# Kernel tuning notes

Hardware: AMD Instinct MI355X
Metric: run time of the kernel (lower is better)

## Reference

```python
import jax, jax.numpy as jnp
import numpy as np
from jax import lax

B, T, C = 32, 4096, 128
CLAMP_LO, CLAMP_HI = 1e-4, 1.0 - 1e-4
LOGIT_ALPHA0 = 0.0                 # logit(0.5)
LOGIT_BETA0 = float(np.log(0.1 / 0.9))  # logit(0.1)


def setup_inputs() -> dict:
    key = jax.random.key(0)
    x = jax.random.normal(key, (B, T, C), dtype=jnp.float32)
    logit_alpha = jnp.full((C,), LOGIT_ALPHA0, dtype=jnp.float32)
    logit_beta = jnp.full((C,), LOGIT_BETA0, dtype=jnp.float32)
    return {"x": x, "logit_alpha": logit_alpha, "logit_beta": logit_beta}


def reference(x, logit_alpha, logit_beta):
    # Holt level+slope exponential smoothing; output is the level series.
    a = jnp.clip(jax.nn.sigmoid(logit_alpha), CLAMP_LO, CLAMP_HI).astype(x.dtype)  # [C]
    b = jnp.clip(jax.nn.sigmoid(logit_beta), CLAMP_LO, CLAMP_HI).astype(x.dtype)   # [C]

    L0 = x[:, 0, :]                       # [B, C]
    slope0 = jnp.zeros_like(L0)

    def step(carry, xt):
        L_prev, slope = carry
        pred = L_prev + slope
        L = pred + a * (xt - pred)
        slope = slope + b * (L - L_prev - slope)
        return (L, slope), L

    xs = jnp.moveaxis(x[:, 1:, :], 1, 0)  # [T-1, B, C], time-major for scan
    _, Ls = lax.scan(step, (L0, slope0), xs)
    out = jnp.concatenate([L0[:, None, :], jnp.moveaxis(Ls, 0, 1)], axis=1)  # [B, T, C]
    return out
```

## Files before the change

kernel.cpp:

```cpp
#include <hip/hip_runtime.h>
#include <math.h>


#define B_ 32
#define T_ 4096
#define C_ 128
#define K_ 64
#define S_ (T_ / K_)
#define C2 (C_ / 2)
#define NCHUNK (B_ * K_)
#define BATCH 16

typedef float v2f __attribute__((ext_vector_type(2)));

__device__ __forceinline__ float sig_clamp(float z) {
    float s = 1.0f / (1.0f + expf(-z));
    return fminf(fmaxf(s, 1.0e-4f), 1.0f - 1.0e-4f);
}

#define STEP(xv0, xv1)                                   \
    {                                                    \
        const float p0 = L0 + sl0;                       \
        const float p1 = L1 + sl1;                       \
        const float g0 = a0 * ((xv0) - p0);              \
        const float g1 = a1 * ((xv1) - p1);              \
        L0 = p0 + g0;  sl0 = fmaf(b0, g0, sl0);          \
        L1 = p1 + g1;  sl1 = fmaf(b1, g1, sl1);          \
    }

__global__ __launch_bounds__(256, 2) void p1_offsets(
        const float* __restrict__ x,
        const float* __restrict__ logit_alpha,
        const float* __restrict__ logit_beta,
        float4* __restrict__ w) {
    const int tid = threadIdx.x & 63;
    const int chunk = blockIdx.x * 4 + (threadIdx.x >> 6);
    const int b = chunk >> 6;
    const int k = chunk & (K_ - 1);

    const float2 la2 = ((const float2*)logit_alpha)[tid];
    const float2 lb2 = ((const float2*)logit_beta)[tid];
    const float a0 = sig_clamp(la2.x), a1 = sig_clamp(la2.y);
    const float b0 = sig_clamp(lb2.x), b1 = sig_clamp(lb2.y);

    const float2* xp = (const float2*)x + ((size_t)b * T_ + (size_t)k * S_) * C2 + tid;

    float2 buf[BATCH];
    float L0, sl0 = 0.0f, L1, sl1 = 0.0f;

    #pragma unroll
    for (int i = 0; i < BATCH; ++i) buf[i] = xp[(size_t)i * C2];
    if (k == 0) { L0 = buf[0].x; L1 = buf[0].y; }
    else        { L0 = 0.0f;     L1 = 0.0f;     }
    #pragma unroll
    for (int i = 0; i < BATCH; ++i) STEP(buf[i].x, buf[i].y);

    for (int base = BATCH; base < S_; base += BATCH) {
        #pragma unroll
        for (int i = 0; i < BATCH; ++i) buf[i] = xp[(size_t)(base + i) * C2];
        #pragma unroll
        for (int i = 0; i < BATCH; ++i) STEP(buf[i].x, buf[i].y);
    }

    w[(size_t)chunk * 64 + tid] = make_float4(L0, sl0, L1, sl1);
}

__global__ __launch_bounds__(256, 2) void p2_emit(
        const float* __restrict__ x,
        const float* __restrict__ logit_alpha,
        const float* __restrict__ logit_beta,
        const float4* __restrict__ w,
        float* __restrict__ out) {
    const int tid = threadIdx.x & 63;
    const int chunk = (NCHUNK - 1) - (blockIdx.x * 4 + (threadIdx.x >> 6));
    const int b = chunk >> 6;
    const int k = chunk & (K_ - 1);

    const float2 la2 = ((const float2*)logit_alpha)[tid];
    const float2 lb2 = ((const float2*)logit_beta)[tid];
    const float a0 = sig_clamp(la2.x), a1 = sig_clamp(la2.y);
    const float b0 = sig_clamp(lb2.x), b1 = sig_clamp(lb2.y);

    const size_t off = ((size_t)b * T_ + (size_t)k * S_) * C2 + tid;
    const v2f* xp = (const v2f*)x + off;
    v2f* op = (v2f*)out + off;

    float L0, sl0 = 0.0f, L1, sl1 = 0.0f;

    if (k > 0) {
        float m00_0 = 1.0f - a0, m01_0 = 1.0f - a0;
        float m10_0 = -a0 * b0,  m11_0 = 1.0f - a0 * b0;
        float m00_1 = 1.0f - a1, m01_1 = 1.0f - a1;
        float m10_1 = -a1 * b1,  m11_1 = 1.0f - a1 * b1;
        #pragma unroll
        for (int i = 0; i < 6; ++i) {
            float n00 = m00_0 * m00_0 + m01_0 * m10_0;
            float n01 = m00_0 * m01_0 + m01_0 * m11_0;
            float n10 = m10_0 * m00_0 + m11_0 * m10_0;
            float n11 = m10_0 * m01_0 + m11_0 * m11_0;
            m00_0 = n00; m01_0 = n01; m10_0 = n10; m11_0 = n11;
            n00 = m00_1 * m00_1 + m01_1 * m10_1;
            n01 = m00_1 * m01_1 + m01_1 * m11_1;
            n10 = m10_1 * m00_1 + m11_1 * m10_1;
            n11 = m10_1 * m01_1 + m11_1 * m11_1;
            m00_1 = n00; m01_1 = n01; m10_1 = n10; m11_1 = n11;
        }
        const float4* wp = w + (size_t)(chunk - k) * 64 + tid;
        float4 s = wp[0];
        #pragma unroll 8
        for (int j = 1; j < k; ++j) {
            const float4 wj = wp[(size_t)j * 64];
            const float nx = m00_0 * s.x + m01_0 * s.y + wj.x;
            const float ny = m10_0 * s.x + m11_0 * s.y + wj.y;
            const float nz = m00_1 * s.z + m01_1 * s.w + wj.z;
            const float nw = m10_1 * s.z + m11_1 * s.w + wj.w;
            s = make_float4(nx, ny, nz, nw);
        }
        L0 = s.x; sl0 = s.y; L1 = s.z; sl1 = s.w;
    }

    v2f buf[BATCH];

    #pragma unroll
    for (int i = 0; i < BATCH; ++i)
        buf[i] = __builtin_nontemporal_load(&xp[(size_t)i * C2]);
    if (k == 0) { L0 = buf[0].x; L1 = buf[0].y; sl0 = 0.0f; sl1 = 0.0f; }
    #pragma unroll
    for (int i = 0; i < BATCH; ++i) {
        STEP(buf[i].x, buf[i].y);
        v2f o; o.x = L0; o.y = L1;
        __builtin_nontemporal_store(o, &op[(size_t)i * C2]);
    }

    for (int base = BATCH; base < S_; base += BATCH) {
        #pragma unroll
        for (int i = 0; i < BATCH; ++i)
            buf[i] = __builtin_nontemporal_load(&xp[(size_t)(base + i) * C2]);
        #pragma unroll
        for (int i = 0; i < BATCH; ++i) {
            STEP(buf[i].x, buf[i].y);
            v2f o; o.x = L0; o.y = L1;
            __builtin_nontemporal_store(o, &op[(size_t)(base + i) * C2]);
        }
    }
}

__global__ void seq_fallback(
        const float* __restrict__ x,
        const float* __restrict__ logit_alpha,
        const float* __restrict__ logit_beta,
        float* __restrict__ out) {
    const int tid = blockIdx.x * blockDim.x + threadIdx.x;
    if (tid >= B_ * C_) return;
    const int b = tid / C_;
    const int c = tid % C_;
    const float a0 = sig_clamp(logit_alpha[c]);
    const float b0 = sig_clamp(logit_beta[c]);
    const float* xp = x + (size_t)b * T_ * C_ + c;
    float* op = out + (size_t)b * T_ * C_ + c;
    float L0 = xp[0], sl0 = 0.0f;
    op[0] = L0;
    for (int t = 1; t < T_; ++t) {
        const float xv = xp[(size_t)t * C_];
        const float p0 = L0 + sl0;
        const float g0 = a0 * (xv - p0);
        L0 = p0 + g0;
        sl0 = fmaf(b0, g0, sl0);
        op[(size_t)t * C_] = L0;
    }
}

extern "C" void kernel_launch(void* const* d_in, const int* in_sizes, int n_in,
                              void* d_out, int out_size, void* d_ws, size_t ws_size,
                              hipStream_t stream) {
    const float* x  = (const float*)d_in[0];
    const float* la = (const float*)d_in[1];
    const float* lb = (const float*)d_in[2];
    float* out = (float*)d_out;

    const size_t need = (size_t)NCHUNK * 64 * sizeof(float4);

    if (ws_size >= need) {
        float4* w = (float4*)d_ws;
        p1_offsets<<<NCHUNK / 4, 256, 0, stream>>>(x, la, lb, w);
        p2_emit<<<NCHUNK / 4, 256, 0, stream>>>(x, la, lb, w, out);
    } else {
        seq_fallback<<<(B_ * C_ + 255) / 256, 256, 0, stream>>>(x, la, lb, out);
    }
}
```

Before: 126.9 us.

## Compute chunk carry-in prefix once per batch in a separate kernel

Adds a small p1b_prefix kernel that runs the chunk-boundary state recurrence once per batch row and writes every chunk's incoming level/slope state to a second workspace slab. Before, each chunk in p2_emit redid the full prefix combine from chunk 0, which is quadratic in the chunk count and caused load imbalance. p2_emit now loads a single precomputed state, so its chunks can run in natural order. The cost is an extra kernel launch, a serial 64-step chain on only 32 blocks, and a doubled workspace requirement.

```diff
diff --git a/kernel.cpp b/kernel.cpp
--- a/kernel.cpp
+++ b/kernel.cpp
@@ -65,59 +65,76 @@
     w[(size_t)chunk * 64 + tid] = make_float4(L0, sl0, L1, sl1);
 }
 
-__global__ __launch_bounds__(256, 2) void p2_emit(
-        const float* __restrict__ x,
+__global__ __launch_bounds__(64) void p1b_prefix(
         const float* __restrict__ logit_alpha,
         const float* __restrict__ logit_beta,
         const float4* __restrict__ w,
-        float* __restrict__ out) {
-    const int tid = threadIdx.x & 63;
-    const int chunk = (NCHUNK - 1) - (blockIdx.x * 4 + (threadIdx.x >> 6));
-    const int b = chunk >> 6;
-    const int k = chunk & (K_ - 1);
+        float4* __restrict__ w2) {
+    const int tid = threadIdx.x;
+    const int b = blockIdx.x;
 
     const float2 la2 = ((const float2*)logit_alpha)[tid];
     const float2 lb2 = ((const float2*)logit_beta)[tid];
     const float a0 = sig_clamp(la2.x), a1 = sig_clamp(la2.y);
     const float b0 = sig_clamp(lb2.x), b1 = sig_clamp(lb2.y);
 
+    float m00_0 = 1.0f - a0, m01_0 = 1.0f - a0;
+    float m10_0 = -a0 * b0,  m11_0 = 1.0f - a0 * b0;
+    float m00_1 = 1.0f - a1, m01_1 = 1.0f - a1;
+    float m10_1 = -a1 * b1,  m11_1 = 1.0f - a1 * b1;
+    #pragma unroll
+    for (int i = 0; i < 6; ++i) {
+        float n00 = m00_0 * m00_0 + m01_0 * m10_0;
+        float n01 = m00_0 * m01_0 + m01_0 * m11_0;
+        float n10 = m10_0 * m00_0 + m11_0 * m10_0;
+        float n11 = m10_0 * m01_0 + m11_0 * m11_0;
+        m00_0 = n00; m01_0 = n01; m10_0 = n10; m11_0 = n11;
+        n00 = m00_1 * m00_1 + m01_1 * m10_1;
+        n01 = m00_1 * m01_1 + m01_1 * m11_1;
+        n10 = m10_1 * m00_1 + m11_1 * m10_1;
+        n11 = m10_1 * m01_1 + m11_1 * m11_1;
+        m00_1 = n00; m01_1 = n01; m10_1 = n10; m11_1 = n11;
+    }
+
+    const float4* wp = w  + ((size_t)b * K_) * 64 + tid;
+    float4*       qp = w2 + ((size_t)b * K_) * 64 + tid;
+
+    float4 s = wp[0];
+    qp[64] = s;
+    #pragma unroll 8
+    for (int k = 2; k < K_; ++k) {
+        const float4 wj = wp[(size_t)(k - 1) * 64];
+        const float nx = m00_0 * s.x + m01_0 * s.y + wj.x;
+        const float ny = m10_0 * s.x + m11_0 * s.y + wj.y;
+        const float nz = m00_1 * s.z + m01_1 * s.w + wj.z;
+        const float nw = m10_1 * s.z + m11_1 * s.w + wj.w;
+        s = make_float4(nx, ny, nz, nw);
+        qp[(size_t)k * 64] = s;
+    }
+}
+
+__global__ __launch_bounds__(256, 2) void p2_emit(
+        const float* __restrict__ x,
+        const float* __restrict__ logit_alpha,
+        const float* __restrict__ logit_beta,
+        const float4* __restrict__ w2,
+        float* __restrict__ out) {
+    const int tid = threadIdx.x & 63;
+    const int chunk = blockIdx.x * 4 + (threadIdx.x >> 6);
+    const int b = chunk >> 6;
+    const int k = chunk & (K_ - 1);
+
+    const float2 la2 = ((const float2*)logit_alpha)[tid];
+    const float2 lb2 = ((const float2*)logit_beta)[tid];
+    const float a0 = sig_clamp(la2.x), a1 = sig_clamp(la2.y);
+    const float b0 = sig_clamp(lb2.x), b1 = sig_clamp(lb2.y);
+
     const size_t off = ((size_t)b * T_ + (size_t)k * S_) * C2 + tid;
     const v2f* xp = (const v2f*)x + off;
     v2f* op = (v2f*)out + off;
 
-    float L0, sl0 = 0.0f, L1, sl1 = 0.0f;
-
-    if (k > 0) {
-        float m00_0 = 1.0f - a0, m01_0 = 1.0f - a0;
-        float m10_0 = -a0 * b0,  m11_0 = 1.0f - a0 * b0;
-        float m00_1 = 1.0f - a1, m01_1 = 1.0f - a1;
-        float m10_1 = -a1 * b1,  m11_1 = 1.0f - a1 * b1;
-        #pragma unroll
-        for (int i = 0; i < 6; ++i) {
-            float n00 = m00_0 * m00_0 + m01_0 * m10_0;
-            float n01 = m00_0 * m01_0 + m01_0 * m11_0;
-            float n10 = m10_0 * m00_0 + m11_0 * m10_0;
-            float n11 = m10_0 * m01_0 + m11_0 * m11_0;
-            m00_0 = n00; m01_0 = n01; m10_0 = n10; m11_0 = n11;
-            n00 = m00_1 * m00_1 + m01_1 * m10_1;
-            n01 = m00_1 * m01_1 + m01_1 * m11_1;
-            n10 = m10_1 * m00_1 + m11_1 * m10_1;
-            n11 = m10_1 * m01_1 + m11_1 * m11_1;
-            m00_1 = n00; m01_1 = n01; m10_1 = n10; m11_1 = n11;
-        }
-        const float4* wp = w + (size_t)(chunk - k) * 64 + tid;
-        float4 s = wp[0];
-        #pragma unroll 8
-        for (int j = 1; j < k; ++j) {
-            const float4 wj = wp[(size_t)j * 64];
-            const float nx = m00_0 * s.x + m01_0 * s.y + wj.x;
-            const float ny = m10_0 * s.x + m11_0 * s.y + wj.y;
-            const float nz = m00_1 * s.z + m01_1 * s.w + wj.z;
-            const float nw = m10_1 * s.z + m11_1 * s.w + wj.w;
-            s = make_float4(nx, ny, nz, nw);
-        }
-        L0 = s.x; sl0 = s.y; L1 = s.z; sl1 = s.w;
-    }
+    const float4 s0 = w2[(size_t)chunk * 64 + tid];
+    float L0 = s0.x, sl0 = s0.y, L1 = s0.z, sl1 = s0.w;
 
     v2f buf[BATCH];
 
@@ -178,12 +195,15 @@
     const float* lb = (const float*)d_in[2];
     float* out = (float*)d_out;
 
-    const size_t need = (size_t)NCHUNK * 64 * sizeof(float4);
+    const size_t slab = (size_t)NCHUNK * 64 * sizeof(float4);
+    const size_t need = 2 * slab;
 
     if (ws_size >= need) {
-        float4* w = (float4*)d_ws;
+        float4* w  = (float4*)d_ws;
+        float4* w2 = w + (size_t)NCHUNK * 64;
         p1_offsets<<<NCHUNK / 4, 256, 0, stream>>>(x, la, lb, w);
-        p2_emit<<<NCHUNK / 4, 256, 0, stream>>>(x, la, lb, w, out);
+        p1b_prefix<<<B_, 64, 0, stream>>>(la, lb, w, w2);
+        p2_emit<<<NCHUNK / 4, 256, 0, stream>>>(x, la, lb, w2, out);
     } else {
         seq_fallback<<<(B_ * C_ + 255) / 256, 256, 0, stream>>>(x, la, lb, out);
     }
```

New measurement: 130.2 us. +2.6%, slower.
